# Kernel optimization log

Hardware: AMD Instinct MI355X
Metric: run time of the kernel (lower is better)

The kernel has to match this reference:

```python
import jax, jax.numpy as jnp
import numpy as np

BETA = 0.01
EPS = 1e-6

def conv3x3(x, w, b):
    y = jax.lax.conv_general_dilated(x, w, (1, 1), 'SAME',
                                     dimension_numbers=('NCHW', 'OIHW', 'NCHW'))
    return y + b[None, :, None, None]

def variance_depth_flow(gt, patch, max_depth):
    B, C, H, W = gt.shape
    py, px = H // patch, W // patch
    # [B,C,py,px,P,P]
    p = gt.reshape(B, C, py, patch, px, patch).transpose(0, 1, 2, 4, 3, 5)
    p = jnp.where((p > 0.1) & (p < max_depth), p, jnp.zeros_like(p))
    bn = jnp.log(p[..., 0, :] + EPS)   # north border  [B,C,py,px,P]
    bs = jnp.log(p[..., -1, :] + EPS)  # south
    bw = jnp.log(p[..., :, 0] + EPS)   # west
    be = jnp.log(p[..., :, -1] + EPS)  # east
    def sx(b):  # shift patches left along x (axis=3), zero-pad last column
        return jnp.concatenate([b[:, :, :, 1:], jnp.zeros_like(b[:, :, :, :1])], axis=3)
    def sy(b):  # shift patches up along y (axis=2), zero-pad last row
        return jnp.concatenate([b[:, :, 1:], jnp.zeros_like(b[:, :, :1])], axis=2)
    diffs = [be - sx(bw), bs - sy(bn), be - sx(be), bs - sy(bs), bw - sx(bw),
             bn - sy(bn), bs - sx(bs), be - sy(be), bn - sx(bn), bw - sy(bw)]
    d = jnp.stack([x.sum(-1) for x in diffs], axis=-1)  # [B,C,py,px,10]
    d = d[:, 0].transpose(0, 3, 1, 2) / patch            # [B,10,py,px]
    return d

def smooth_l1(pred, target, beta):
    d = pred - target
    ad = jnp.abs(d)
    return jnp.where(ad < beta, 0.5 * d * d / beta, ad - 0.5 * beta)

def setup_inputs() -> dict:
    key = jax.random.key(0)
    ks = jax.random.split(key, 7)
    B, FC, DC, hw, HW = 32, 256, 64, 64, 512
    feat = jax.random.normal(ks[0], (B, FC, hw, hw), dtype=jnp.float32)
    depth = jax.random.normal(ks[1], (B, DC, hw, hw), dtype=jnp.float32)
    gts = jax.random.uniform(ks[2], (B, 1, HW, HW), dtype=jnp.float32)
    W_att = jax.random.normal(ks[3], (DC, FC, 3, 3), dtype=jnp.float32) * 0.02
    b_att = jnp.zeros((DC,), dtype=jnp.float32)
    W_post = jax.random.normal(ks[4], (10, DC, 3, 3), dtype=jnp.float32) * 0.05
    b_post = jnp.zeros((10,), dtype=jnp.float32)
    return {"feat": feat, "depth": depth, "gts": gts,
            "W_att": W_att, "b_att": b_att, "W_post": W_post, "b_post": b_post}

def reference(feat, depth, gts, W_att, b_att, W_post, b_post):
    max_depth = 80.0
    n, c, h, w = depth.shape
    patch = gts.shape[2] // h
    flow_gradient = variance_depth_flow(gts, patch, max_depth)  # [B,10,h,w]
    att = jax.nn.sigmoid(conv3x3(feat, W_att, b_att))           # [B,DC,h,w]
    ds = conv3x3(att * depth, W_post, b_post)                   # [B,10,h,w]
    diff = smooth_l1(ds, flow_gradient, BETA)
    return diff.sum() / (h * w * ds.shape[0] * ds.shape[1])
```

## Files before the change

### kernel.cpp

```cpp
#include <hip/hip_runtime.h>
#include <hip/hip_bf16.h>


typedef __attribute__((ext_vector_type(4))) float f32x4;
typedef __attribute__((ext_vector_type(8))) short s16x8;

#define DEVFN __device__ __forceinline__

DEVFN float bf2f(unsigned short u){
  unsigned int x = ((unsigned int)u) << 16;
  float f; __builtin_memcpy(&f, &x, 4); return f;
}
DEVFN unsigned short f2bf(float f){
  unsigned int x; __builtin_memcpy(&x, &f, 4);
  x += 0x7fffu + ((x >> 16) & 1u);
  return (unsigned short)(x >> 16);
}

#define ASYNC16(gp, lp) __builtin_amdgcn_global_load_lds( \
    (const __attribute__((address_space(1))) unsigned int*)(gp), \
    (__attribute__((address_space(3))) unsigned int*)(lp), 16, 0, 0)

__global__ void k_weights(const float* __restrict__ Watt, const float* __restrict__ Wpost,
                          unsigned short* __restrict__ WT1, unsigned short* __restrict__ WT2){
  const int t = blockIdx.x * 256 + threadIdx.x;
  const int n1 = 9 * 64 * 256;
  if (t < n1){
    const int tap = t / (64 * 256);
    const int rem = t % (64 * 256);
    const int oc = rem / 256, ic = rem % 256;
    WT1[t] = f2bf(Watt[(oc * 256 + ic) * 9 + tap]);
  }
  const int n2 = 9 * 16 * 64;
  if (t < n2){
    const int tap = t / (16 * 64);
    const int rem = t % (16 * 64);
    const int od = rem / 64, ic = rem % 64;
    const float v = (od < 10) ? Wpost[(od * 64 + ic) * 9 + tap] : 0.0f;
    WT2[t] = f2bf(v);
  }
}

__global__ void k_borders(const float* __restrict__ gts, float* __restrict__ S,
                          float* __restrict__ out){
  const int bid = blockIdx.x, tid = threadIdx.x;
  if (bid == 0 && tid == 0) *out = 0.0f;
  __shared__ float slab[4096];
  const int rel = bid;
  const float* gp = gts + (size_t)rel * 4096;
#pragma unroll
  for (int it = 0; it < 4; ++it){
    const int id = it * 256 + tid;
    *(f32x4*)&slab[id * 4] = *(const f32x4*)&gp[id * 4];
  }
  __syncthreads();
  const int px = tid & 63, border = tid >> 6;
  float s = 0.0f;
#pragma unroll
  for (int i = 0; i < 8; ++i){
    float v;
    if (border == 0)      v = slab[px * 8 + i];
    else if (border == 1) v = slab[7 * 512 + px * 8 + i];
    else if (border == 2) v = slab[i * 512 + px * 8];
    else                  v = slab[i * 512 + px * 8 + 7];
    v = ((v > 0.1f) && (v < 80.0f)) ? v : 0.0f;
    s += __logf(v + 1e-6f);
  }
  S[((size_t)rel * 64 + px) * 4 + border] = s;
}

__global__ __launch_bounds__(512, 2) void k_gemm1(
    const float* __restrict__ feat,
    const unsigned short* __restrict__ WT1,
    const float* __restrict__ batt,
    const float* __restrict__ depth,
    unsigned short* __restrict__ adT)
{
  __shared__ unsigned short As[720 * 32];
  __shared__ unsigned short Bs[2][576 * 32];
  const int t = threadIdx.x;
  const int l = t & 63, w = t >> 6;
  const int b = blockIdx.x >> 3, ytile = blockIdx.x & 7;
  const int y0 = ytile * 8;
  const int fr = l & 15, g = l >> 4;
  const int x = t & 63, seg = t >> 6;

  f32x4 acc[4][4];
#pragma unroll
  for (int i = 0; i < 4; ++i)
#pragma unroll
    for (int j = 0; j < 4; ++j)
#pragma unroll
      for (int q = 0; q < 4; ++q) acc[i][j][q] = 0.0f;

  if (t < 80){
    const int yy = t >> 3, k = t & 7;
    const int xp = (k & 1) ? 65 : 0;
    s16x8 z = {0,0,0,0,0,0,0,0};
    *(s16x8*)&As[(yy * 72 + xp) * 32 + (k >> 1) * 8] = z;
  }

  auto stageB = [&](int c, int d){
#pragma unroll
    for (int it = 0; it < 5; ++it){
      const int idx = it * 512 + t;
      if (idx < 2304){
        const int row = idx >> 2;
        const int sg = (idx & 3) ^ ((row >> 1) & 3);
        ASYNC16(WT1 + (size_t)row * 256 + c * 32 + sg * 8, &Bs[d][(size_t)idx * 8]);
      }
    }
  };
  auto loadA = [&](int c, float* rr){
#pragma unroll
    for (int j = 0; j < 5; ++j){
      const int idx = seg + j * 8;
      const int yy = idx >> 2, icg = idx & 3;
      const int yr = y0 - 1 + yy;
      if (yr >= 0 && yr < 64){
        const float* gp = feat + ((size_t)(b * 256 + c * 32 + icg * 8)) * 4096
                               + (size_t)yr * 64 + x;
#pragma unroll
        for (int e = 0; e < 8; ++e) rr[j * 8 + e] = gp[(size_t)e * 4096];
      } else {
#pragma unroll
        for (int e = 0; e < 8; ++e) rr[j * 8 + e] = 0.0f;
      }
    }
  };
  auto cvtA = [&](const float* rr, s16x8* vA){
#pragma unroll
    for (int j = 0; j < 5; ++j)
#pragma unroll
      for (int e = 0; e < 8; ++e) vA[j][e] = (short)f2bf(rr[j * 8 + e]);
  };
  auto writeA = [&](const s16x8* vA){
    const int xp = x + 1;
    const int sx = (xp >> 1) & 3;
#pragma unroll
    for (int j = 0; j < 5; ++j){
      const int idx = seg + j * 8;
      const int yy = idx >> 2, icg = idx & 3;
      *(s16x8*)&As[(yy * 72 + xp) * 32 + ((icg ^ sx) * 8)] = vA[j];
    }
  };
  auto compute = [&](const unsigned short* Bb, int t0, int t1){
    const int slotB = (g ^ ((fr >> 1) & 3)) * 8;
    for (int tap = t0; tap < t1; ++tap){
      const int dy = tap / 3 - 1, dxp = tap % 3;
      const int r = fr + dxp;
      const int slotA = (g ^ ((r >> 1) & 3)) * 8;
      const int rowb = ((w + dy + 1) * 72 + r) * 32 + slotA;
      s16x8 af[4], bfr[4];
#pragma unroll
      for (int i = 0; i < 4; ++i) af[i] = *(const s16x8*)&As[rowb + i * 512];
#pragma unroll
      for (int j = 0; j < 4; ++j)
        bfr[j] = *(const s16x8*)&Bb[(tap * 64 + j * 16 + fr) * 32 + slotB];
#pragma unroll
      for (int i = 0; i < 4; ++i)
#pragma unroll
        for (int j = 0; j < 4; ++j)
          acc[i][j] = __builtin_amdgcn_mfma_f32_16x16x32_bf16(af[i], bfr[j], acc[i][j], 0, 0, 0);
    }
  };

  float rr[40]; s16x8 vA[5];
  stageB(0, 0);
  loadA(0, rr);
  cvtA(rr, vA);
  writeA(vA);
  __syncthreads();

  for (int c = 0; c < 8; ++c){
    const int cur = c & 1;
    if (c < 7){ stageB(c + 1, cur ^ 1); loadA(c + 1, rr); }
    compute(Bs[cur], 0, 5);
    if (c < 7) cvtA(rr, vA);
    compute(Bs[cur], 5, 9);
    __syncthreads();
    if (c < 7) writeA(vA);
    __syncthreads();
  }

  const int y = y0 + w;
#pragma unroll
  for (int j = 0; j < 4; ++j){
    const int oc = j * 16 + fr;
    const float bb = batt[oc];
    const float* dpt = depth + ((size_t)(b * 64 + oc)) * 4096 + (size_t)y * 64;
    unsigned short* op = adT + ((size_t)(b * 4096 + y * 64)) * 64 + oc;
#pragma unroll
    for (int i = 0; i < 4; ++i){
#pragma unroll
      for (int q = 0; q < 4; ++q){
        const int xo = i * 16 + g * 4 + q;
        const float v = acc[i][j][q] + bb;
        const float att = 1.0f / (1.0f + __expf(-v));
        op[(size_t)xo * 64] = f2bf(att * dpt[xo]);
      }
    }
  }
}

DEVFN float sel4(f32x4 v, int i){
  const float ab = (i & 1) ? v[1] : v[0];
  const float cd = (i & 1) ? v[3] : v[2];
  return (i & 2) ? cd : ab;
}

__global__ __launch_bounds__(512, 2) void k_gemm2(
    const unsigned short* __restrict__ adT,
    const unsigned short* __restrict__ WT2,
    const float* __restrict__ bpost,
    const f32x4* __restrict__ S,
    float* __restrict__ out)
{
  __shared__ unsigned short As[2][20480];
  __shared__ unsigned short Bs[9216];
  __shared__ float ps[8];
  const int t = threadIdx.x;
  const int l = t & 63, w = t >> 6;
  const int b = blockIdx.x >> 3, ytile = blockIdx.x & 7;
  const int y0 = ytile * 8;
  const int fr = l & 15, g = l >> 4;

  f32x4 acc[4];
#pragma unroll
  for (int i = 0; i < 4; ++i)
#pragma unroll
    for (int q = 0; q < 4; ++q) acc[i][q] = 0.0f;

  auto stageA = [&](int c, int d){
#pragma unroll
    for (int it2 = 0; it2 < 5; ++it2){
      const int it = it2 * 2 + (t >> 8);
      const int yy = y0 - 1 + it;
      const int xx = (t >> 2) & 63, icg = t & 3;
      unsigned short* lp = &As[d][(it * 64 + xx) * 32 + icg * 8];
      if (yy >= 0 && yy < 64){
        const int sg = icg ^ ((xx >> 1) & 3);
        const unsigned short* gp = adT
            + ((size_t)(b * 4096 + yy * 64 + xx)) * 64 + c * 32 + sg * 8;
        ASYNC16(gp, lp);
      } else {
        s16x8 z = {0,0,0,0,0,0,0,0};
        *(s16x8*)lp = z;
      }
    }
  };
#pragma unroll
  for (int it = 0; it < 3; ++it){
    const int idx = it * 512 + t;
    if (idx < 1152){
      const int row = idx >> 3, p = idx & 7;
      const int sg = p ^ (row & 7);
      ASYNC16(WT2 + (size_t)row * 64 + sg * 8, Bs + (size_t)idx * 8);
    }
  }
  stageA(0, 0);
  __syncthreads();

  for (int c = 0; c < 2; ++c){
    if (c == 0) stageA(1, 1);
    const unsigned short* Ab = As[c];
    const int pB = ((c * 4 + g) ^ (fr & 7)) * 8;
    for (int tap = 0; tap < 9; ++tap){
      const int dy = tap / 3 - 1, dx = tap % 3 - 1;
      s16x8 af[4];
#pragma unroll
      for (int i = 0; i < 4; ++i){
        const int xv = i * 16 + fr + dx;
        const bool valid = (xv >= 0) && (xv < 64);
        const int xw = valid ? xv : 0;
        const int slot = (g ^ ((xw >> 1) & 3)) * 8;
        s16x8 v = *(const s16x8*)&Ab[((w + dy + 1) * 64 + xw) * 32 + slot];
        s16x8 z = {0,0,0,0,0,0,0,0};
        af[i] = valid ? v : z;
      }
      const s16x8 bfr = *(const s16x8*)&Bs[(tap * 16 + fr) * 64 + pB];
#pragma unroll
      for (int i = 0; i < 4; ++i)
        acc[i] = __builtin_amdgcn_mfma_f32_16x16x32_bf16(af[i], bfr, acc[i], 0, 0, 0);
    }
    __syncthreads();
  }

  const unsigned aPack = (3u<<0)|(1u<<2)|(3u<<4)|(1u<<6)|(2u<<8)|(0u<<10)|(1u<<12)|(3u<<14)|(0u<<16)|(2u<<18);
  const unsigned bPack = (2u<<0)|(0u<<2)|(3u<<4)|(1u<<6)|(2u<<8)|(0u<<10)|(1u<<12)|(3u<<14)|(0u<<16)|(2u<<18);
  float lsum = 0.0f;
  const int y = y0 + w;
  if (fr < 10){
    const int od = fr;
    const int ai = (aPack >> (2 * od)) & 3;
    const int bi = (bPack >> (2 * od)) & 3;
    const bool xshift = (od & 1) == 0;
    const float bp = bpost[od];
#pragma unroll
    for (int i = 0; i < 4; ++i){
#pragma unroll
      for (int q = 0; q < 4; ++q){
        const int xo = i * 16 + g * 4 + q;
        const size_t gm = (size_t)b * 4096 + (size_t)y * 64 + xo;
        const f32x4 sa = S[gm];
        const bool nb = xshift ? (xo < 63) : (y < 63);
        const size_t ga = xshift ? (nb ? gm + 1 : gm) : (nb ? gm + 64 : gm);
        const f32x4 sbv = S[ga];
        const float sbf = nb ? sel4(sbv, bi) : 0.0f;
        const float flow = (sel4(sa, ai) - sbf) * 0.125f;
        const float dv = acc[i][q] + bp - flow;
        const float adv = fabsf(dv);
        lsum += (adv < 0.01f) ? (50.0f * dv * dv) : (adv - 0.005f);
      }
    }
  }
#pragma unroll
  for (int off = 32; off > 0; off >>= 1) lsum += __shfl_down(lsum, off);
  if (l == 0) ps[w] = lsum;
  __syncthreads();
  if (t == 0){
    float s = 0.0f;
#pragma unroll
    for (int i = 0; i < 8; ++i) s += ps[i];
    atomicAdd(out, s * (1.0f / 1310720.0f));
  }
}

extern "C" void kernel_launch(void* const* d_in, const int* in_sizes, int n_in,
                              void* d_out, int out_size, void* d_ws, size_t ws_size,
                              hipStream_t stream){
  const float* feat  = (const float*)d_in[0];
  const float* depth = (const float*)d_in[1];
  const float* gts   = (const float*)d_in[2];
  const float* Watt  = (const float*)d_in[3];
  const float* batt  = (const float*)d_in[4];
  const float* Wpost = (const float*)d_in[5];
  const float* bpost = (const float*)d_in[6];
  float* out = (float*)d_out;
  char* ws = (char*)d_ws;

  unsigned short* adT = (unsigned short*)ws;
  unsigned short* WT1 = (unsigned short*)(ws + 16777216);
  unsigned short* WT2 = (unsigned short*)(ws + 16777216 + 294912);
  float*          S   = (float*)(ws + 16777216 + 294912 + 18432);

  k_weights<<<576, 256, 0, stream>>>(Watt, Wpost, WT1, WT2);
  k_gemm1<<<256, 512, 0, stream>>>(feat, WT1, batt, depth, adT);
  k_borders<<<2048, 256, 0, stream>>>(gts, S, out);
  k_gemm2<<<256, 512, 0, stream>>>(adT, WT2, bpost, (const f32x4*)S, out);
}
```

Baseline: 89.03 us.

## Shrink conv1 GEMM tiles to 4 rows and drop double-buffered prefetch

k_gemm1 now uses 256-thread blocks that each cover 4 output rows instead of 8, launched as 512 blocks. The double-buffered weight staging and the register prefetch of the next channel chunk are replaced by a simple load, sync, compute loop with a single B buffer. The goal is a much smaller LDS footprint so more blocks fit per CU and latency is hidden by occupancy rather than software pipelining. In exchange, each weight chunk is loaded by twice as many blocks, and loads no longer overlap MFMA work inside a block.

New measurement: 90.16 us. About the same (+1.3%).

```diff
diff --git a/kernel.cpp b/kernel.cpp
--- a/kernel.cpp
+++ b/kernel.cpp
@@ -69,21 +69,21 @@
   S[((size_t)rel * 64 + px) * 4 + border] = s;
 }
 
-__global__ __launch_bounds__(512, 2) void k_gemm1(
+__global__ __launch_bounds__(256, 2) void k_gemm1(
     const float* __restrict__ feat,
     const unsigned short* __restrict__ WT1,
     const float* __restrict__ batt,
     const float* __restrict__ depth,
     unsigned short* __restrict__ adT)
 {
-  __shared__ unsigned short As[720 * 32];
-  __shared__ unsigned short Bs[2][576 * 32];
+  __shared__ unsigned short As[6 * 66 * 32];
+  __shared__ unsigned short Bs[576 * 32];
   const int t = threadIdx.x;
   const int l = t & 63, w = t >> 6;
-  const int b = blockIdx.x >> 3, ytile = blockIdx.x & 7;
-  const int y0 = ytile * 8;
+  const int b = blockIdx.x >> 4, ytile = blockIdx.x & 15;
+  const int y0 = ytile * 4;
   const int fr = l & 15, g = l >> 4;
-  const int x = t & 63, seg = t >> 6;
+  const int x = l;
 
   f32x4 acc[4][4];
 #pragma unroll
@@ -93,32 +93,24 @@
 #pragma unroll
       for (int q = 0; q < 4; ++q) acc[i][j][q] = 0.0f;
 
-  if (t < 80){
+  if (t < 48){
     const int yy = t >> 3, k = t & 7;
     const int xp = (k & 1) ? 65 : 0;
     s16x8 z = {0,0,0,0,0,0,0,0};
-    *(s16x8*)&As[(yy * 72 + xp) * 32 + (k >> 1) * 8] = z;
-  }
-
-  auto stageB = [&](int c, int d){
-#pragma unroll
-    for (int it = 0; it < 5; ++it){
-      const int idx = it * 512 + t;
-      if (idx < 2304){
-        const int row = idx >> 2;
-        const int sg = (idx & 3) ^ ((row >> 1) & 3);
-        ASYNC16(WT1 + (size_t)row * 256 + c * 32 + sg * 8, &Bs[d][(size_t)idx * 8]);
-      }
-    }
-  };
-  auto loadA = [&](int c, float* rr){
-#pragma unroll
-    for (int j = 0; j < 5; ++j){
-      const int idx = seg + j * 8;
-      const int yy = idx >> 2, icg = idx & 3;
-      const int yr = y0 - 1 + yy;
+    *(s16x8*)&As[(yy * 66 + xp) * 32 + (k >> 1) * 8] = z;
+  }
+
+  const int xp = x + 1;
+  const int sx = (xp >> 1) & 3;
+  const int slotB = (g ^ ((fr >> 1) & 3)) * 8;
+
+  for (int c = 0; c < 8; ++c){
+    float rr[48];
+#pragma unroll
+    for (int j = 0; j < 6; ++j){
+      const int yr = y0 - 1 + j;
       if (yr >= 0 && yr < 64){
-        const float* gp = feat + ((size_t)(b * 256 + c * 32 + icg * 8)) * 4096
+        const float* gp = feat + ((size_t)(b * 256 + c * 32 + w * 8)) * 4096
                                + (size_t)yr * 64 + x;
 #pragma unroll
         for (int e = 0; e < 8; ++e) rr[j * 8 + e] = gp[(size_t)e * 4096];
@@ -127,59 +119,39 @@
         for (int e = 0; e < 8; ++e) rr[j * 8 + e] = 0.0f;
       }
     }
-  };
-  auto cvtA = [&](const float* rr, s16x8* vA){
-#pragma unroll
-    for (int j = 0; j < 5; ++j)
-#pragma unroll
-      for (int e = 0; e < 8; ++e) vA[j][e] = (short)f2bf(rr[j * 8 + e]);
-  };
-  auto writeA = [&](const s16x8* vA){
-    const int xp = x + 1;
-    const int sx = (xp >> 1) & 3;
-#pragma unroll
-    for (int j = 0; j < 5; ++j){
-      const int idx = seg + j * 8;
-      const int yy = idx >> 2, icg = idx & 3;
-      *(s16x8*)&As[(yy * 72 + xp) * 32 + ((icg ^ sx) * 8)] = vA[j];
-    }
-  };
-  auto compute = [&](const unsigned short* Bb, int t0, int t1){
-    const int slotB = (g ^ ((fr >> 1) & 3)) * 8;
-    for (int tap = t0; tap < t1; ++tap){
+#pragma unroll
+    for (int it = 0; it < 9; ++it){
+      const int idx = it * 256 + t;
+      const int row = idx >> 2;
+      const int sg = (idx & 3) ^ ((row >> 1) & 3);
+      ASYNC16(WT1 + (size_t)row * 256 + c * 32 + sg * 8, &Bs[(size_t)idx * 8]);
+    }
+#pragma unroll
+    for (int j = 0; j < 6; ++j){
+      s16x8 v;
+#pragma unroll
+      for (int e = 0; e < 8; ++e) v[e] = (short)f2bf(rr[j * 8 + e]);
+      *(s16x8*)&As[(j * 66 + xp) * 32 + ((w ^ sx) * 8)] = v;
+    }
+    __syncthreads();
+
+    for (int tap = 0; tap < 9; ++tap){
       const int dy = tap / 3 - 1, dxp = tap % 3;
       const int r = fr + dxp;
       const int slotA = (g ^ ((r >> 1) & 3)) * 8;
-      const int rowb = ((w + dy + 1) * 72 + r) * 32 + slotA;
+      const int rowb = ((w + dy + 1) * 66 + r) * 32 + slotA;
       s16x8 af[4], bfr[4];
 #pragma unroll
       for (int i = 0; i < 4; ++i) af[i] = *(const s16x8*)&As[rowb + i * 512];
 #pragma unroll
       for (int j = 0; j < 4; ++j)
-        bfr[j] = *(const s16x8*)&Bb[(tap * 64 + j * 16 + fr) * 32 + slotB];
+        bfr[j] = *(const s16x8*)&Bs[(tap * 64 + j * 16 + fr) * 32 + slotB];
 #pragma unroll
       for (int i = 0; i < 4; ++i)
 #pragma unroll
         for (int j = 0; j < 4; ++j)
           acc[i][j] = __builtin_amdgcn_mfma_f32_16x16x32_bf16(af[i], bfr[j], acc[i][j], 0, 0, 0);
     }
-  };
-
-  float rr[40]; s16x8 vA[5];
-  stageB(0, 0);
-  loadA(0, rr);
-  cvtA(rr, vA);
-  writeA(vA);
-  __syncthreads();
-
-  for (int c = 0; c < 8; ++c){
-    const int cur = c & 1;
-    if (c < 7){ stageB(c + 1, cur ^ 1); loadA(c + 1, rr); }
-    compute(Bs[cur], 0, 5);
-    if (c < 7) cvtA(rr, vA);
-    compute(Bs[cur], 5, 9);
-    __syncthreads();
-    if (c < 7) writeA(vA);
     __syncthreads();
   }
 
@@ -345,7 +317,7 @@
   float*          S   = (float*)(ws + 16777216 + 294912 + 18432);
 
   k_weights<<<576, 256, 0, stream>>>(Watt, Wpost, WT1, WT2);
-  k_gemm1<<<256, 512, 0, stream>>>(feat, WT1, batt, depth, adT);
+  k_gemm1<<<512, 256, 0, stream>>>(feat, WT1, batt, depth, adT);
   k_borders<<<2048, 256, 0, stream>>>(gts, S, out);
   k_gemm2<<<256, 512, 0, stream>>>(adT, WT2, bpost, (const f32x4*)S, out);
 }
```
